# Optimization experiments

Hardware: AMD Instinct MI355X
Metric: run time of the kernel (lower is better)

Reference implementation:

```python
import jax, jax.numpy as jnp
import numpy as np
import math

D_MODEL = 1024
N_HEAD = 16
D_K = D_MODEL // N_HEAD
NEG_INF = -1e30  # fp32 mask fill value used by the torch module


def _rope(x, b_rotate=None):
    # x: [b, h, n, k], k even. Interleaved (even/odd) RoPE, matching the torch code.
    b, h, n, k = x.shape
    half = k // 2
    inv_freq = 1.0 / (10000.0 ** (jnp.arange(half, dtype=jnp.float32) / half))  # [half]
    ang = jnp.arange(n, dtype=jnp.float32)[:, None] * inv_freq[None, :]          # [n, half]
    sin = jnp.sin(ang)
    cos = jnp.cos(ang)
    x1 = x[..., 0::2]  # [b,h,n,half]
    x2 = x[..., 1::2]
    even = x1 * cos - x2 * sin
    odd = x1 * sin + x2 * cos
    out = jnp.stack([even, odd], axis=-1).reshape(b, h, n, k)  # re-interleave
    if b_rotate is not None:
        out = out * b_rotate  # barope multiplicative term
    return out


def setup_inputs() -> dict:
    key = jax.random.key(0)
    ks = jax.random.split(key, 7)
    B, S = 1, 2048
    query = jax.random.normal(ks[0], (B, S, D_MODEL), dtype=jnp.float32)
    kk = jax.random.normal(ks[1], (B, S, D_MODEL), dtype=jnp.float32)
    value = jax.random.normal(ks[2], (B, S, D_MODEL), dtype=jnp.float32)
    b_emb = jax.random.normal(ks[3], (B, S, D_MODEL), dtype=jnp.float32)
    mask = jax.random.bernoulli(ks[4], 0.9, (B, S))  # bool [B,S]
    linear_layers = 0.02 * jax.random.normal(ks[5], (3, D_MODEL, N_HEAD, D_K), dtype=jnp.float32)
    b_proj = jax.random.normal(ks[6], (D_MODEL, N_HEAD, D_K), dtype=jnp.float32)
    return {"query": query, "key": kk, "value": value, "b_emb": b_emb,
            "mask": mask, "linear_layers": linear_layers, "b_proj": b_proj}


def reference(query, key, value, b_emb, mask, linear_layers, b_proj):
    B, S, _ = query.shape
    # QKV projections: [b,n,d] x [d,h,k] -> [b,h,n,k]
    q = jnp.einsum('bnd,dhk->bhnk', query, linear_layers[0])
    k = jnp.einsum('bnd,dhk->bhnk', key, linear_layers[1])
    v = jnp.einsum('bnd,dhk->bhnk', value, linear_layers[2])
    # barope=True branch: multiplicative rotation modifier from b_emb
    b_rotate = jnp.einsum('bnd,dhk->bhnk', b_emb, b_proj)
    q = _rope(q, b_rotate)
    k = _rope(k, b_rotate)
    scores = jnp.einsum('bhqk,bhmk->bhqm', q, k) / math.sqrt(D_K)  # [b,h,s,s]
    pair_mask = (mask[:, :, None] & mask[:, None, :])[:, None]     # [b,1,s,s]
    scores = jnp.where(pair_mask, scores, NEG_INF)
    p_attn = jax.nn.softmax(scores, axis=-1)  # dropout p=0 -> identity
    x = jnp.einsum('bhqm,bhmk->bhqk', p_attn, v)
    return x.transpose(0, 2, 1, 3).reshape(B, S, N_HEAD * D_K)
```

## Files before the change

### kernel.cpp

```cpp
#include <hip/hip_runtime.h>
#include <hip/hip_bf16.h>
#include <math.h>

#define S_LEN 2048
#define NHEAD 16
#define DMODEL 1024

typedef short bf16x8 __attribute__((ext_vector_type(8)));
typedef float f32x4 __attribute__((ext_vector_type(4)));

static __device__ __forceinline__ unsigned short bfbits(float x) {
    __hip_bfloat16 h = __float2bfloat16(x);
    unsigned short u; __builtin_memcpy(&u, &h, 2); return u;
}
static __device__ __forceinline__ float bf2f(unsigned short u) {
    union { unsigned int i; float f; } v; v.i = ((unsigned int)u) << 16; return v.f;
}
static __device__ __forceinline__ void splitRN(float x, unsigned short& hi, unsigned short& lo) {
    unsigned short h = bfbits(x);
    float r = x - bf2f(h);
    hi = h; lo = bfbits(r);
}
static __device__ __forceinline__ void split4(float4 x, ushort4& h4, ushort4& l4) {
    unsigned short h0,l0,h1,l1,h2,l2,h3,l3;
    splitRN(x.x,h0,l0); splitRN(x.y,h1,l1); splitRN(x.z,h2,l2); splitRN(x.w,h3,l3);
    h4 = make_ushort4(h0,h1,h2,h3); l4 = make_ushort4(l0,l1,l2,l3);
}

__device__ __forceinline__ int mask_at(const void* mp, int enc, int s) {
    if (enc) return ((const unsigned char*)mp)[s] != 0;
    return ((const unsigned int*)mp)[s] != 0u;
}

__global__ void detect_kernel(const void* __restrict__ mask, int* __restrict__ flags) {
    if (threadIdx.x == 0 && blockIdx.x == 0) {
        const unsigned int* m = (const unsigned int*)mask;
        int bytey = 0;
        for (int i = 0; i < 8; ++i) {
            unsigned int u = m[i];
            if (u != 0u && u != 1u && u != 0x3F800000u) bytey = 1;
        }
        flags[0] = bytey;
    }
}

__global__ __launch_bounds__(256)
void presplit_w(const float* __restrict__ ll, const float* __restrict__ bproj,
                unsigned short* __restrict__ Wh, unsigned short* __restrict__ Wl) {
    __shared__ unsigned short Th[64][72], Tl[64][72];
    const int t = threadIdx.x;
    const int bid = blockIdx.x;
    const int stream = bid >> 8;
    const int rem = bid & 255;
    const int h = rem >> 4;
    const int d0 = (rem & 15) << 6;
    const float* src = (stream == 3) ? bproj : (ll + (size_t)stream * 1048576);
#pragma unroll
    for (int rep = 0; rep < 4; ++rep) {
        int fid = rep * 256 + t;
        int dl = fid >> 4, n4 = (fid & 15) * 4;
        float4 w = *(const float4*)&src[(size_t)(d0 + dl) * 1024 + h * 64 + n4];
        unsigned short hh, lo2;
#pragma unroll
        for (int m = 0; m < 4; ++m) { splitRN((&w.x)[m], hh, lo2); Th[n4+m][dl] = hh; Tl[n4+m][dl] = lo2; }
    }
    __syncthreads();
    size_t obase = (size_t)stream * 1048576;
#pragma unroll
    for (int rep = 0; rep < 2; ++rep) {
        int wid = rep * 256 + t;
        int n = wid >> 3, dl8 = (wid & 7) * 8;
        int dtile = n >> 4, cc = n & 15;
        int dglob = d0 + dl8;
        int kc = dglob >> 5;
        int qd = (dglob >> 3) & 3;
        size_t off = obase + (size_t)(h * 4 + dtile) * 16384 + (size_t)kc * 512
                   + (size_t)(qd * 16 + cc) * 8;
        *(uint4*)&Wh[off] = *(uint4*)&Th[n][dl8];
        *(uint4*)&Wl[off] = *(uint4*)&Tl[n][dl8];
    }
}

__global__ __launch_bounds__(256, 4)
void proj_fused5(const float* __restrict__ Xq, const float* __restrict__ Xk,
                 const float* __restrict__ Xv, const float* __restrict__ Xb,
                 const unsigned short* __restrict__ Wh, const unsigned short* __restrict__ Wl,
                 unsigned short* __restrict__ qhi, unsigned short* __restrict__ qlo,
                 unsigned short* __restrict__ khi, unsigned short* __restrict__ klo,
                 unsigned short* __restrict__ vhi) {
    __shared__ unsigned short smem[8960];
    unsigned short (*XQh)[40] = (unsigned short(*)[40])(smem + 0 * 1280);
    unsigned short (*XQl)[40] = (unsigned short(*)[40])(smem + 1 * 1280);
    unsigned short (*XKh)[40] = (unsigned short(*)[40])(smem + 2 * 1280);
    unsigned short (*XKl)[40] = (unsigned short(*)[40])(smem + 3 * 1280);
    unsigned short (*XVh)[40] = (unsigned short(*)[40])(smem + 4 * 1280);
    unsigned short (*XBh)[40] = (unsigned short(*)[40])(smem + 5 * 1280);
    unsigned short (*XBl)[40] = (unsigned short(*)[40])(smem + 6 * 1280);
    unsigned short (*T0)[72] = (unsigned short(*)[72])(smem + 0);
    unsigned short (*T1)[72] = (unsigned short(*)[72])(smem + 2304);
    unsigned short (*T2)[40] = (unsigned short(*)[40])(smem + 4608);

    const int t = threadIdx.x;
    const int lin = blockIdx.x;
    const int xcd = lin & 7;
    const int inner = lin >> 3;
    const int h = inner >> 3;
    const int sg = inner & 7;
    const int s0 = (xcd * 8 + sg) * 32;
    const int lane = t & 63, dt = t >> 6, quad = lane >> 4, c = lane & 15;

    f32x4 aq[2], ak[2], av[2], ab[2];
#pragma unroll
    for (int i = 0; i < 2; ++i) {
        aq[i] = (f32x4){0.f,0.f,0.f,0.f}; ak[i] = (f32x4){0.f,0.f,0.f,0.f};
        av[i] = (f32x4){0.f,0.f,0.f,0.f}; ab[i] = (f32x4){0.f,0.f,0.f,0.f};
    }

    const int xr = t >> 3, xc = (t & 7) * 4;
    const size_t xg = (size_t)(s0 + xr) * DMODEL + xc;
    const size_t wb = (size_t)(h * 4 + dt) * 16384 + (size_t)lane * 8;

    float4 pq, pk, pv, pb;
    pq = *(const float4*)&Xq[xg];
    pk = *(const float4*)&Xk[xg];
    pv = *(const float4*)&Xv[xg];
    pb = *(const float4*)&Xb[xg];

    for (int kc = 0; kc < 32; ++kc) {
        __syncthreads();
        {
            ushort4 h4, l4;
            split4(pq, h4, l4); *(ushort4*)&XQh[xr][xc] = h4; *(ushort4*)&XQl[xr][xc] = l4;
            split4(pk, h4, l4); *(ushort4*)&XKh[xr][xc] = h4; *(ushort4*)&XKl[xr][xc] = l4;
            split4(pb, h4, l4); *(ushort4*)&XBh[xr][xc] = h4; *(ushort4*)&XBl[xr][xc] = l4;
            *(ushort4*)&XVh[xr][xc] = make_ushort4(bfbits(pv.x),bfbits(pv.y),bfbits(pv.z),bfbits(pv.w));
        }
        __syncthreads();

        size_t wo = wb + (size_t)kc * 512;
        bf16x8 aQh = *(const bf16x8*)&Wh[wo];
        bf16x8 aQl = *(const bf16x8*)&Wl[wo];
        bf16x8 aKh = *(const bf16x8*)&Wh[1048576 + wo];
        bf16x8 aKl = *(const bf16x8*)&Wl[1048576 + wo];
        bf16x8 aVh = *(const bf16x8*)&Wh[2097152 + wo];
        bf16x8 aVl = *(const bf16x8*)&Wl[2097152 + wo];
        bf16x8 aBh = *(const bf16x8*)&Wh[3145728 + wo];
        bf16x8 aBl = *(const bf16x8*)&Wl[3145728 + wo];

        if (kc + 1 < 32) {
            size_t g = xg + (size_t)(kc + 1) * 32;
            pq = *(const float4*)&Xq[g];
            pk = *(const float4*)&Xk[g];
            pv = *(const float4*)&Xv[g];
            pb = *(const float4*)&Xb[g];
        }

#pragma unroll
        for (int st = 0; st < 2; ++st) {
            bf16x8 b1 = *(bf16x8*)&XQh[st*16+c][quad*8];
            bf16x8 b2 = *(bf16x8*)&XQl[st*16+c][quad*8];
            aq[st] = __builtin_amdgcn_mfma_f32_16x16x32_bf16(aQh, b1, aq[st], 0, 0, 0);
            aq[st] = __builtin_amdgcn_mfma_f32_16x16x32_bf16(aQh, b2, aq[st], 0, 0, 0);
            aq[st] = __builtin_amdgcn_mfma_f32_16x16x32_bf16(aQl, b1, aq[st], 0, 0, 0);
            aq[st] = __builtin_amdgcn_mfma_f32_16x16x32_bf16(aQl, b2, aq[st], 0, 0, 0);
            b1 = *(bf16x8*)&XKh[st*16+c][quad*8];
            b2 = *(bf16x8*)&XKl[st*16+c][quad*8];
            ak[st] = __builtin_amdgcn_mfma_f32_16x16x32_bf16(aKh, b1, ak[st], 0, 0, 0);
            ak[st] = __builtin_amdgcn_mfma_f32_16x16x32_bf16(aKh, b2, ak[st], 0, 0, 0);
            ak[st] = __builtin_amdgcn_mfma_f32_16x16x32_bf16(aKl, b1, ak[st], 0, 0, 0);
            ak[st] = __builtin_amdgcn_mfma_f32_16x16x32_bf16(aKl, b2, ak[st], 0, 0, 0);
            b1 = *(bf16x8*)&XVh[st*16+c][quad*8];
            av[st] = __builtin_amdgcn_mfma_f32_16x16x32_bf16(aVh, b1, av[st], 0, 0, 0);
            av[st] = __builtin_amdgcn_mfma_f32_16x16x32_bf16(aVl, b1, av[st], 0, 0, 0);
            b1 = *(bf16x8*)&XBh[st*16+c][quad*8];
            b2 = *(bf16x8*)&XBl[st*16+c][quad*8];
            ab[st] = __builtin_amdgcn_mfma_f32_16x16x32_bf16(aBh, b1, ab[st], 0, 0, 0);
            ab[st] = __builtin_amdgcn_mfma_f32_16x16x32_bf16(aBh, b2, ab[st], 0, 0, 0);
            ab[st] = __builtin_amdgcn_mfma_f32_16x16x32_bf16(aBl, b1, ab[st], 0, 0, 0);
            ab[st] = __builtin_amdgcn_mfma_f32_16x16x32_bf16(aBl, b2, ab[st], 0, 0, 0);
        }
    }

    float rq[2][4], rk[2][4];
    {
        int p0 = dt * 8 + 2 * quad;
        double inv0 = pow(10000.0, -(double)p0 / 32.0);
        double inv1 = pow(10000.0, -(double)(p0 + 1) / 32.0);
#pragma unroll
        for (int st = 0; st < 2; ++st) {
            int s = s0 + st * 16 + c;
            double a0 = (double)s * inv0, a1 = (double)s * inv1;
            float sn0 = (float)sin(a0), cs0 = (float)cos(a0);
            float sn1 = (float)sin(a1), cs1 = (float)cos(a1);
            rq[st][0] = (aq[st][0]*cs0 - aq[st][1]*sn0) * ab[st][0];
            rq[st][1] = (aq[st][0]*sn0 + aq[st][1]*cs0) * ab[st][1];
            rq[st][2] = (aq[st][2]*cs1 - aq[st][3]*sn1) * ab[st][2];
            rq[st][3] = (aq[st][2]*sn1 + aq[st][3]*cs1) * ab[st][3];
            rk[st][0] = (ak[st][0]*cs0 - ak[st][1]*sn0) * ab[st][0];
            rk[st][1] = (ak[st][0]*sn0 + ak[st][1]*cs0) * ab[st][1];
            rk[st][2] = (ak[st][2]*cs1 - ak[st][3]*sn1) * ab[st][2];
            rk[st][3] = (ak[st][2]*sn1 + ak[st][3]*cs1) * ab[st][3];
        }
    }
    __syncthreads();
#pragma unroll
    for (int st = 0; st < 2; ++st) {
        unsigned short h0,l0,h1,l1,h2,l2,h3,l3;
        splitRN(rq[st][0],h0,l0); splitRN(rq[st][1],h1,l1);
        splitRN(rq[st][2],h2,l2); splitRN(rq[st][3],h3,l3);
        *(ushort4*)&T0[st*16+c][dt*16+4*quad] = make_ushort4(h0,h1,h2,h3);
        *(ushort4*)&T1[st*16+c][dt*16+4*quad] = make_ushort4(l0,l1,l2,l3);
#pragma unroll
        for (int reg = 0; reg < 4; ++reg)
            T2[dt * 16 + 4 * quad + reg][st * 16 + c] = bfbits(av[st][reg]);
    }
    __syncthreads();
    {
        int row = t >> 3, d8 = (t & 7) * 8;
        size_t qb = ((size_t)(h * S_LEN + s0 + row)) * 64 + d8;
        *(uint4*)&qhi[qb] = *(uint4*)&T0[row][d8];
        *(uint4*)&qlo[qb] = *(uint4*)&T1[row][d8];
        int d = t >> 2, s8 = (t & 3) * 8;
        size_t vb = ((size_t)(h * 64 + d)) * S_LEN + s0 + s8;
        *(uint4*)&vhi[vb] = *(uint4*)&T2[d][s8];
    }
    __syncthreads();
#pragma unroll
    for (int st = 0; st < 2; ++st) {
        unsigned short h0,l0,h1,l1,h2,l2,h3,l3;
        splitRN(rk[st][0],h0,l0); splitRN(rk[st][1],h1,l1);
        splitRN(rk[st][2],h2,l2); splitRN(rk[st][3],h3,l3);
        *(ushort4*)&T0[st*16+c][dt*16+4*quad] = make_ushort4(h0,h1,h2,h3);
        *(ushort4*)&T1[st*16+c][dt*16+4*quad] = make_ushort4(l0,l1,l2,l3);
    }
    __syncthreads();
    {
        int row = t >> 3, d8 = (t & 7) * 8;
        size_t qb = ((size_t)(h * S_LEN + s0 + row)) * 64 + d8;
        *(uint4*)&khi[qb] = *(uint4*)&T0[row][d8];
        *(uint4*)&klo[qb] = *(uint4*)&T1[row][d8];
    }
}

__global__ __launch_bounds__(256)
void attn_mfma(const unsigned short* __restrict__ qh, const unsigned short* __restrict__ ql,
               const unsigned short* __restrict__ kh, const unsigned short* __restrict__ kl,
               const unsigned short* __restrict__ vh,
               const void* __restrict__ mask, float* __restrict__ out,
               const int* __restrict__ flags) {
    __shared__ unsigned short Kh[2][64][72], Kl[2][64][72];
    __shared__ unsigned short Vt[2][64][72];
    __shared__ unsigned short Sh[64][72], Sl[64][72];
    const int menc = flags[0];
    const int t = threadIdx.x;
    const int lin = blockIdx.x + (blockIdx.y << 5);
    const int h = (lin & 7) * 2 + ((lin >> 3) & 1);
    const int s0 = (lin >> 4) * 64;
    const int lane = t & 63, w = t >> 6, quad = lane >> 4, c = lane & 15;

    bf16x8 qfh[2], qfl[2];
#pragma unroll
    for (int ks = 0; ks < 2; ++ks) {
        size_t base = ((size_t)(h * S_LEN + s0 + 16 * w + c)) * 64 + ks * 32 + quad * 8;
        qfh[ks] = *(const bf16x8*)&qh[base];
        qfl[ks] = *(const bf16x8*)&ql[base];
    }
    int mq[4];
#pragma unroll
    for (int i = 0; i < 4; ++i) mq[i] = mask_at(mask, menc, s0 + 16 * w + quad * 4 + i);

    float m_i[4], l_i[4];
#pragma unroll
    for (int i = 0; i < 4; ++i) { m_i[i] = -INFINITY; l_i[i] = 0.0f; }
    f32x4 o_acc[4];
#pragma unroll
    for (int i = 0; i < 4; ++i) o_acc[i] = (f32x4){0.f,0.f,0.f,0.f};

    uint4 pre[6];
#pragma unroll
    for (int i = 0; i < 2; ++i) {
        int id = i * 256 + t, row = id >> 3, col8 = (id & 7) * 8;
        size_t kb = ((size_t)(h * S_LEN + row)) * 64 + col8;
        size_t vb = ((size_t)(h * 64 + row)) * S_LEN + col8;
        pre[0 + i] = *(const uint4*)&kh[kb];
        pre[2 + i] = *(const uint4*)&kl[kb];
        pre[4 + i] = *(const uint4*)&vh[vb];
    }
#pragma unroll
    for (int i = 0; i < 2; ++i) {
        int id = i * 256 + t, row = id >> 3, col8 = (id & 7) * 8;
        *(uint4*)&Kh[0][row][col8] = pre[0 + i];
        *(uint4*)&Kl[0][row][col8] = pre[2 + i];
        *(uint4*)&Vt[0][row][col8] = pre[4 + i];
    }
    __syncthreads();

    int cur = 0;
    for (int kt = 0; kt < 32; ++kt) {
        if (kt + 1 < 32) {
            const int kb0 = (kt + 1) * 64;
#pragma unroll
            for (int i = 0; i < 2; ++i) {
                int id = i * 256 + t, row = id >> 3, col8 = (id & 7) * 8;
                size_t kb = ((size_t)(h * S_LEN + kb0 + row)) * 64 + col8;
                size_t vb = ((size_t)(h * 64 + row)) * S_LEN + kb0 + col8;
                pre[0 + i] = *(const uint4*)&kh[kb];
                pre[2 + i] = *(const uint4*)&kl[kb];
                pre[4 + i] = *(const uint4*)&vh[vb];
            }
        }
        int mk[4];
#pragma unroll
        for (int nt = 0; nt < 4; ++nt) mk[nt] = mask_at(mask, menc, kt * 64 + 16 * nt + c);

        f32x4 sc[4];
#pragma unroll
        for (int i = 0; i < 4; ++i) sc[i] = (f32x4){0.f,0.f,0.f,0.f};
#pragma unroll
        for (int nt = 0; nt < 4; ++nt)
#pragma unroll
            for (int ks = 0; ks < 2; ++ks) {
                bf16x8 kfh = *(bf16x8*)&Kh[cur][nt * 16 + c][ks * 32 + quad * 8];
                bf16x8 kfl = *(bf16x8*)&Kl[cur][nt * 16 + c][ks * 32 + quad * 8];
                sc[nt] = __builtin_amdgcn_mfma_f32_16x16x32_bf16(qfh[ks], kfh, sc[nt], 0, 0, 0);
                sc[nt] = __builtin_amdgcn_mfma_f32_16x16x32_bf16(qfh[ks], kfl, sc[nt], 0, 0, 0);
                sc[nt] = __builtin_amdgcn_mfma_f32_16x16x32_bf16(qfl[ks], kfh, sc[nt], 0, 0, 0);
            }

        float sm[4][4];
#pragma unroll
        for (int nt = 0; nt < 4; ++nt)
#pragma unroll
            for (int reg = 0; reg < 4; ++reg)
                sm[nt][reg] = (mq[reg] && mk[nt]) ? sc[nt][reg] * 0.125f : -1e30f;

        float rmax[4];
#pragma unroll
        for (int reg = 0; reg < 4; ++reg)
            rmax[reg] = fmaxf(fmaxf(sm[0][reg], sm[1][reg]), fmaxf(sm[2][reg], sm[3][reg]));
#pragma unroll
        for (int off = 1; off <= 8; off <<= 1)
#pragma unroll
            for (int reg = 0; reg < 4; ++reg)
                rmax[reg] = fmaxf(rmax[reg], __shfl_xor(rmax[reg], off, 64));

        float mn[4], alpha[4];
#pragma unroll
        for (int reg = 0; reg < 4; ++reg) {
            mn[reg] = fmaxf(m_i[reg], rmax[reg]);
            alpha[reg] = __expf(m_i[reg] - mn[reg]);
            m_i[reg] = mn[reg];
        }

        float rsum[4] = {0.f, 0.f, 0.f, 0.f};
#pragma unroll
        for (int nt = 0; nt < 4; ++nt)
#pragma unroll
            for (int reg = 0; reg < 4; ++reg) {
                float e = __expf(sm[nt][reg] - mn[reg]);
                rsum[reg] += e;
                unsigned short eh, el;
                splitRN(e, eh, el);
                Sh[16 * w + quad * 4 + reg][16 * nt + c] = eh;
                Sl[16 * w + quad * 4 + reg][16 * nt + c] = el;
            }
#pragma unroll
        for (int off = 1; off <= 8; off <<= 1)
#pragma unroll
            for (int reg = 0; reg < 4; ++reg)
                rsum[reg] += __shfl_xor(rsum[reg], off, 64);
#pragma unroll
        for (int reg = 0; reg < 4; ++reg) l_i[reg] = l_i[reg] * alpha[reg] + rsum[reg];
        if (!__all(alpha[0] == 1.0f && alpha[1] == 1.0f &&
                   alpha[2] == 1.0f && alpha[3] == 1.0f)) {
#pragma unroll
            for (int nt = 0; nt < 4; ++nt)
#pragma unroll
                for (int reg = 0; reg < 4; ++reg) o_acc[nt][reg] *= alpha[reg];
        }

        if (kt + 1 < 32) {
            const int nxt = cur ^ 1;
#pragma unroll
            for (int i = 0; i < 2; ++i) {
                int id = i * 256 + t, row = id >> 3, col8 = (id & 7) * 8;
                *(uint4*)&Kh[nxt][row][col8] = pre[0 + i];
                *(uint4*)&Kl[nxt][row][col8] = pre[2 + i];
                *(uint4*)&Vt[nxt][row][col8] = pre[4 + i];
            }
        }

#pragma unroll
        for (int ks = 0; ks < 2; ++ks) {
            bf16x8 pfh = *(bf16x8*)&Sh[16 * w + c][ks * 32 + quad * 8];
            bf16x8 pfl = *(bf16x8*)&Sl[16 * w + c][ks * 32 + quad * 8];
#pragma unroll
            for (int nt = 0; nt < 4; ++nt) {
                bf16x8 vf = *(bf16x8*)&Vt[cur][nt * 16 + c][ks * 32 + quad * 8];
                o_acc[nt] = __builtin_amdgcn_mfma_f32_16x16x32_bf16(pfh, vf, o_acc[nt], 0, 0, 0);
                o_acc[nt] = __builtin_amdgcn_mfma_f32_16x16x32_bf16(pfl, vf, o_acc[nt], 0, 0, 0);
            }
        }
        __syncthreads();
        cur ^= 1;
    }

#pragma unroll
    for (int reg = 0; reg < 4; ++reg) {
        float inv = 1.0f / l_i[reg];
        int row = s0 + 16 * w + quad * 4 + reg;
#pragma unroll
        for (int nt = 0; nt < 4; ++nt)
            out[(size_t)row * 1024 + h * 64 + nt * 16 + c] = o_acc[nt][reg] * inv;
    }
}

extern "C" void kernel_launch(void* const* d_in, const int* in_sizes, int n_in,
                              void* d_out, int out_size, void* d_ws, size_t ws_size,
                              hipStream_t stream) {
    const float* query = (const float*)d_in[0];
    const float* key   = (const float*)d_in[1];
    const float* value = (const float*)d_in[2];
    const float* b_emb = (const float*)d_in[3];
    const void*  mask  = d_in[4];
    const float* ll    = (const float*)d_in[5];
    const float* bproj = (const float*)d_in[6];
    float* out = (float*)d_out;

    const size_t HSD = (size_t)NHEAD * S_LEN * 64;
    char* ws = (char*)d_ws;
    int* flags = (int*)ws;
    unsigned short* qhi = (unsigned short*)(ws + 4096);
    unsigned short* qlo = qhi + HSD;
    unsigned short* khi = qlo + HSD;
    unsigned short* klo = khi + HSD;
    unsigned short* vhi = klo + HSD;
    unsigned short* Wh  = vhi + HSD;
    unsigned short* Wl  = Wh + 4 * 1048576;

    dim3 pb(256);
    detect_kernel<<<1, 64, 0, stream>>>(mask, flags);
    presplit_w<<<1024, pb, 0, stream>>>(ll, bproj, Wh, Wl);
    proj_fused5<<<1024, pb, 0, stream>>>(query, key, value, b_emb,
                                         Wh, Wl, qhi, qlo, khi, klo, vhi);
    attn_mfma<<<dim3(32, 16), pb, 0, stream>>>(qhi, qlo, khi, klo, vhi, mask, out, flags);
}
```

Baseline: 268.8 us.

## Double-buffer projection LDS tiles, drop lo*lo MFMAs, fold softmax scale into Q

The projection kernel now double-buffers its split-bf16 X tiles in LDS, so there is one barrier per k-step instead of two, and global loads are prefetched two steps ahead. It also drops the lo*lo MFMA term for Q, K and the rotation product, which cuts compute at a small cost in precision. The 1/sqrt(dk) scale is folded into Q after RoPE instead of being applied to every score. In attention, the alpha rescale is now unconditional and an extra barrier is added before the PV MFMAs, which may add sync cost.

```diff
diff --git a/kernel.cpp b/kernel.cpp
--- a/kernel.cpp
+++ b/kernel.cpp
@@ -82,20 +82,13 @@
 }
 
 __global__ __launch_bounds__(256, 4)
-void proj_fused5(const float* __restrict__ Xq, const float* __restrict__ Xk,
+void proj_fused7(const float* __restrict__ Xq, const float* __restrict__ Xk,
                  const float* __restrict__ Xv, const float* __restrict__ Xb,
                  const unsigned short* __restrict__ Wh, const unsigned short* __restrict__ Wl,
                  unsigned short* __restrict__ qhi, unsigned short* __restrict__ qlo,
                  unsigned short* __restrict__ khi, unsigned short* __restrict__ klo,
                  unsigned short* __restrict__ vhi) {
-    __shared__ unsigned short smem[8960];
-    unsigned short (*XQh)[40] = (unsigned short(*)[40])(smem + 0 * 1280);
-    unsigned short (*XQl)[40] = (unsigned short(*)[40])(smem + 1 * 1280);
-    unsigned short (*XKh)[40] = (unsigned short(*)[40])(smem + 2 * 1280);
-    unsigned short (*XKl)[40] = (unsigned short(*)[40])(smem + 3 * 1280);
-    unsigned short (*XVh)[40] = (unsigned short(*)[40])(smem + 4 * 1280);
-    unsigned short (*XBh)[40] = (unsigned short(*)[40])(smem + 5 * 1280);
-    unsigned short (*XBl)[40] = (unsigned short(*)[40])(smem + 6 * 1280);
+    __shared__ unsigned short smem[17920];
     unsigned short (*T0)[72] = (unsigned short(*)[72])(smem + 0);
     unsigned short (*T1)[72] = (unsigned short(*)[72])(smem + 2304);
     unsigned short (*T2)[40] = (unsigned short(*)[40])(smem + 4608);
@@ -120,23 +113,30 @@
     const size_t xg = (size_t)(s0 + xr) * DMODEL + xc;
     const size_t wb = (size_t)(h * 4 + dt) * 16384 + (size_t)lane * 8;
 
+#define XARR(name, b, i) unsigned short (*name)[40] = (unsigned short(*)[40])(smem + (b) * 8960 + (i) * 1280)
+
     float4 pq, pk, pv, pb;
     pq = *(const float4*)&Xq[xg];
     pk = *(const float4*)&Xk[xg];
     pv = *(const float4*)&Xv[xg];
     pb = *(const float4*)&Xb[xg];
+    {
+        XARR(XQh,0,0); XARR(XQl,0,1); XARR(XKh,0,2); XARR(XKl,0,3);
+        XARR(XVh,0,4); XARR(XBh,0,5); XARR(XBl,0,6);
+        ushort4 h4, l4;
+        split4(pq, h4, l4); *(ushort4*)&XQh[xr][xc] = h4; *(ushort4*)&XQl[xr][xc] = l4;
+        split4(pk, h4, l4); *(ushort4*)&XKh[xr][xc] = h4; *(ushort4*)&XKl[xr][xc] = l4;
+        split4(pb, h4, l4); *(ushort4*)&XBh[xr][xc] = h4; *(ushort4*)&XBl[xr][xc] = l4;
+        *(ushort4*)&XVh[xr][xc] = make_ushort4(bfbits(pv.x),bfbits(pv.y),bfbits(pv.z),bfbits(pv.w));
+    }
+    pq = *(const float4*)&Xq[xg + 32];
+    pk = *(const float4*)&Xk[xg + 32];
+    pv = *(const float4*)&Xv[xg + 32];
+    pb = *(const float4*)&Xb[xg + 32];
+    __syncthreads();
 
     for (int kc = 0; kc < 32; ++kc) {
-        __syncthreads();
-        {
-            ushort4 h4, l4;
-            split4(pq, h4, l4); *(ushort4*)&XQh[xr][xc] = h4; *(ushort4*)&XQl[xr][xc] = l4;
-            split4(pk, h4, l4); *(ushort4*)&XKh[xr][xc] = h4; *(ushort4*)&XKl[xr][xc] = l4;
-            split4(pb, h4, l4); *(ushort4*)&XBh[xr][xc] = h4; *(ushort4*)&XBl[xr][xc] = l4;
-            *(ushort4*)&XVh[xr][xc] = make_ushort4(bfbits(pv.x),bfbits(pv.y),bfbits(pv.z),bfbits(pv.w));
-        }
-        __syncthreads();
-
+        const int cb = kc & 1, nb = cb ^ 1;
         size_t wo = wb + (size_t)kc * 512;
         bf16x8 aQh = *(const bf16x8*)&Wh[wo];
         bf16x8 aQl = *(const bf16x8*)&Wl[wo];
@@ -148,38 +148,50 @@
         bf16x8 aBl = *(const bf16x8*)&Wl[3145728 + wo];
 
         if (kc + 1 < 32) {
-            size_t g = xg + (size_t)(kc + 1) * 32;
+            XARR(XQh,nb,0); XARR(XQl,nb,1); XARR(XKh,nb,2); XARR(XKl,nb,3);
+            XARR(XVh,nb,4); XARR(XBh,nb,5); XARR(XBl,nb,6);
+            ushort4 h4, l4;
+            split4(pq, h4, l4); *(ushort4*)&XQh[xr][xc] = h4; *(ushort4*)&XQl[xr][xc] = l4;
+            split4(pk, h4, l4); *(ushort4*)&XKh[xr][xc] = h4; *(ushort4*)&XKl[xr][xc] = l4;
+            split4(pb, h4, l4); *(ushort4*)&XBh[xr][xc] = h4; *(ushort4*)&XBl[xr][xc] = l4;
+            *(ushort4*)&XVh[xr][xc] = make_ushort4(bfbits(pv.x),bfbits(pv.y),bfbits(pv.z),bfbits(pv.w));
+        }
+        if (kc + 2 < 32) {
+            size_t g = xg + (size_t)(kc + 2) * 32;
             pq = *(const float4*)&Xq[g];
             pk = *(const float4*)&Xk[g];
             pv = *(const float4*)&Xv[g];
             pb = *(const float4*)&Xb[g];
         }
 
-#pragma unroll
-        for (int st = 0; st < 2; ++st) {
-            bf16x8 b1 = *(bf16x8*)&XQh[st*16+c][quad*8];
-            bf16x8 b2 = *(bf16x8*)&XQl[st*16+c][quad*8];
-            aq[st] = __builtin_amdgcn_mfma_f32_16x16x32_bf16(aQh, b1, aq[st], 0, 0, 0);
-            aq[st] = __builtin_amdgcn_mfma_f32_16x16x32_bf16(aQh, b2, aq[st], 0, 0, 0);
-            aq[st] = __builtin_amdgcn_mfma_f32_16x16x32_bf16(aQl, b1, aq[st], 0, 0, 0);
-            aq[st] = __builtin_amdgcn_mfma_f32_16x16x32_bf16(aQl, b2, aq[st], 0, 0, 0);
-            b1 = *(bf16x8*)&XKh[st*16+c][quad*8];
-            b2 = *(bf16x8*)&XKl[st*16+c][quad*8];
-            ak[st] = __builtin_amdgcn_mfma_f32_16x16x32_bf16(aKh, b1, ak[st], 0, 0, 0);
-            ak[st] = __builtin_amdgcn_mfma_f32_16x16x32_bf16(aKh, b2, ak[st], 0, 0, 0);
-            ak[st] = __builtin_amdgcn_mfma_f32_16x16x32_bf16(aKl, b1, ak[st], 0, 0, 0);
-            ak[st] = __builtin_amdgcn_mfma_f32_16x16x32_bf16(aKl, b2, ak[st], 0, 0, 0);
-            b1 = *(bf16x8*)&XVh[st*16+c][quad*8];
-            av[st] = __builtin_amdgcn_mfma_f32_16x16x32_bf16(aVh, b1, av[st], 0, 0, 0);
-            av[st] = __builtin_amdgcn_mfma_f32_16x16x32_bf16(aVl, b1, av[st], 0, 0, 0);
-            b1 = *(bf16x8*)&XBh[st*16+c][quad*8];
-            b2 = *(bf16x8*)&XBl[st*16+c][quad*8];
-            ab[st] = __builtin_amdgcn_mfma_f32_16x16x32_bf16(aBh, b1, ab[st], 0, 0, 0);
-            ab[st] = __builtin_amdgcn_mfma_f32_16x16x32_bf16(aBh, b2, ab[st], 0, 0, 0);
-            ab[st] = __builtin_amdgcn_mfma_f32_16x16x32_bf16(aBl, b1, ab[st], 0, 0, 0);
-            ab[st] = __builtin_amdgcn_mfma_f32_16x16x32_bf16(aBl, b2, ab[st], 0, 0, 0);
-        }
-    }
+        {
+            XARR(XQh,cb,0); XARR(XQl,cb,1); XARR(XKh,cb,2); XARR(XKl,cb,3);
+            XARR(XVh,cb,4); XARR(XBh,cb,5); XARR(XBl,cb,6);
+#pragma unroll
+            for (int st = 0; st < 2; ++st) {
+                bf16x8 b1 = *(bf16x8*)&XQh[st*16+c][quad*8];
+                bf16x8 b2 = *(bf16x8*)&XQl[st*16+c][quad*8];
+                aq[st] = __builtin_amdgcn_mfma_f32_16x16x32_bf16(aQh, b1, aq[st], 0, 0, 0);
+                aq[st] = __builtin_amdgcn_mfma_f32_16x16x32_bf16(aQh, b2, aq[st], 0, 0, 0);
+                aq[st] = __builtin_amdgcn_mfma_f32_16x16x32_bf16(aQl, b1, aq[st], 0, 0, 0);
+                b1 = *(bf16x8*)&XKh[st*16+c][quad*8];
+                b2 = *(bf16x8*)&XKl[st*16+c][quad*8];
+                ak[st] = __builtin_amdgcn_mfma_f32_16x16x32_bf16(aKh, b1, ak[st], 0, 0, 0);
+                ak[st] = __builtin_amdgcn_mfma_f32_16x16x32_bf16(aKh, b2, ak[st], 0, 0, 0);
+                ak[st] = __builtin_amdgcn_mfma_f32_16x16x32_bf16(aKl, b1, ak[st], 0, 0, 0);
+                b1 = *(bf16x8*)&XVh[st*16+c][quad*8];
+                av[st] = __builtin_amdgcn_mfma_f32_16x16x32_bf16(aVh, b1, av[st], 0, 0, 0);
+                av[st] = __builtin_amdgcn_mfma_f32_16x16x32_bf16(aVl, b1, av[st], 0, 0, 0);
+                b1 = *(bf16x8*)&XBh[st*16+c][quad*8];
+                b2 = *(bf16x8*)&XBl[st*16+c][quad*8];
+                ab[st] = __builtin_amdgcn_mfma_f32_16x16x32_bf16(aBh, b1, ab[st], 0, 0, 0);
+                ab[st] = __builtin_amdgcn_mfma_f32_16x16x32_bf16(aBh, b2, ab[st], 0, 0, 0);
+                ab[st] = __builtin_amdgcn_mfma_f32_16x16x32_bf16(aBl, b1, ab[st], 0, 0, 0);
+            }
+        }
+        __syncthreads();
+    }
+#undef XARR
 
     float rq[2][4], rk[2][4];
     {
@@ -192,10 +204,10 @@
             double a0 = (double)s * inv0, a1 = (double)s * inv1;
             float sn0 = (float)sin(a0), cs0 = (float)cos(a0);
             float sn1 = (float)sin(a1), cs1 = (float)cos(a1);
-            rq[st][0] = (aq[st][0]*cs0 - aq[st][1]*sn0) * ab[st][0];
-            rq[st][1] = (aq[st][0]*sn0 + aq[st][1]*cs0) * ab[st][1];
-            rq[st][2] = (aq[st][2]*cs1 - aq[st][3]*sn1) * ab[st][2];
-            rq[st][3] = (aq[st][2]*sn1 + aq[st][3]*cs1) * ab[st][3];
+            rq[st][0] = (aq[st][0]*cs0 - aq[st][1]*sn0) * ab[st][0] * 0.125f;
+            rq[st][1] = (aq[st][0]*sn0 + aq[st][1]*cs0) * ab[st][1] * 0.125f;
+            rq[st][2] = (aq[st][2]*cs1 - aq[st][3]*sn1) * ab[st][2] * 0.125f;
+            rq[st][3] = (aq[st][2]*sn1 + aq[st][3]*cs1) * ab[st][3] * 0.125f;
             rk[st][0] = (ak[st][0]*cs0 - ak[st][1]*sn0) * ab[st][0];
             rk[st][1] = (ak[st][0]*sn0 + ak[st][1]*cs0) * ab[st][1];
             rk[st][2] = (ak[st][2]*cs1 - ak[st][3]*sn1) * ab[st][2];
@@ -332,7 +344,7 @@
         for (int nt = 0; nt < 4; ++nt)
 #pragma unroll
             for (int reg = 0; reg < 4; ++reg)
-                sm[nt][reg] = (mq[reg] && mk[nt]) ? sc[nt][reg] * 0.125f : -1e30f;
+                sm[nt][reg] = (mq[reg] && mk[nt]) ? sc[nt][reg] : -1e30f;
 
         float rmax[4];
 #pragma unroll
@@ -371,13 +383,10 @@
                 rsum[reg] += __shfl_xor(rsum[reg], off, 64);
 #pragma unroll
         for (int reg = 0; reg < 4; ++reg) l_i[reg] = l_i[reg] * alpha[reg] + rsum[reg];
-        if (!__all(alpha[0] == 1.0f && alpha[1] == 1.0f &&
-                   alpha[2] == 1.0f && alpha[3] == 1.0f)) {
-#pragma unroll
-            for (int nt = 0; nt < 4; ++nt)
-#pragma unroll
-                for (int reg = 0; reg < 4; ++reg) o_acc[nt][reg] *= alpha[reg];
-        }
+#pragma unroll
+        for (int nt = 0; nt < 4; ++nt)
+#pragma unroll
+            for (int reg = 0; reg < 4; ++reg) o_acc[nt][reg] *= alpha[reg];
 
         if (kt + 1 < 32) {
             const int nxt = cur ^ 1;
@@ -389,6 +398,7 @@
                 *(uint4*)&Vt[nxt][row][col8] = pre[4 + i];
             }
         }
+        __syncthreads();
 
 #pragma unroll
         for (int ks = 0; ks < 2; ++ks) {
@@ -438,10 +448,9 @@
     unsigned short* Wh  = vhi + HSD;
     unsigned short* Wl  = Wh + 4 * 1048576;
 
-    dim3 pb(256);
     detect_kernel<<<1, 64, 0, stream>>>(mask, flags);
-    presplit_w<<<1024, pb, 0, stream>>>(ll, bproj, Wh, Wl);
-    proj_fused5<<<1024, pb, 0, stream>>>(query, key, value, b_emb,
-                                         Wh, Wl, qhi, qlo, khi, klo, vhi);
-    attn_mfma<<<dim3(32, 16), pb, 0, stream>>>(qhi, qlo, khi, klo, vhi, mask, out, flags);
-}
+    presplit_w<<<1024, 256, 0, stream>>>(ll, bproj, Wh, Wl);
+    proj_fused7<<<1024, 256, 0, stream>>>(query, key, value, b_emb,
+                                          Wh, Wl, qhi, qlo, khi, klo, vhi);
+    attn_mfma<<<dim3(32, 16), 256, 0, stream>>>(qhi, qlo, khi, klo, vhi, mask, out, flags);
+}
```

Result: no change. 264.6 us (median of 2 runs) (-1.6%).
